# Performance work log

Measured on AMD Instinct MI355X. Metric: run time of the kernel, lower is better.

Reference implementation:

```python
import jax, jax.numpy as jnp
import numpy as np

C = 512
GROUPS = 32
EPS = 1e-6


def group_norm(x, w, b):
    # x: [B, C, H, W]
    B, Cc, H, W = x.shape
    xg = x.reshape(B, GROUPS, Cc // GROUPS, H, W)
    mean = xg.mean(axis=(2, 3, 4), keepdims=True)
    var = xg.var(axis=(2, 3, 4), keepdims=True)
    xg = (xg - mean) * jax.lax.rsqrt(var + EPS)
    x = xg.reshape(B, Cc, H, W)
    return x * w[None, :, None, None] + b[None, :, None, None]


def conv1x1(x, w, b):
    # 1x1 conv == per-pixel channel matmul; w: [Cout, Cin]
    return jnp.einsum('bchw,oc->bohw', x, w) + b[None, :, None, None]


def setup_inputs() -> dict:
    key = jax.random.key(0)
    ks = jax.random.split(key, 11)
    s = 1.0 / np.sqrt(C)
    d = {
        'x': jax.random.normal(ks[0], (2, C, 64, 64), dtype=jnp.float32),
        'gn_w': jnp.ones((C,), jnp.float32),
        'gn_b': jnp.zeros((C,), jnp.float32),
        'wq': jax.random.normal(ks[1], (C, C), jnp.float32) * s,
        'bq': jax.random.normal(ks[2], (C,), jnp.float32) * 0.01,
        'wk': jax.random.normal(ks[3], (C, C), jnp.float32) * s,
        'bk': jax.random.normal(ks[4], (C,), jnp.float32) * 0.01,
        'wv': jax.random.normal(ks[5], (C, C), jnp.float32) * s,
        'bv': jax.random.normal(ks[6], (C,), jnp.float32) * 0.01,
        'wo': jax.random.normal(ks[7], (C, C), jnp.float32) * s,
        'bo': jax.random.normal(ks[8], (C,), jnp.float32) * 0.01,
    }
    return d


def reference(x, gn_w, gn_b, wq, bq, wk, bk, wv, bv, wo, bo):
    B, Cc, H, W = x.shape
    h = group_norm(x, gn_w, gn_b)
    q = conv1x1(h, wq, bq)  # [B,C,H,W]
    k = conv1x1(h, wk, bk)
    v = conv1x1(h, wv, bv)
    N = H * W
    q = q.reshape(B, Cc, N).transpose(0, 2, 1)   # b n c
    k = k.reshape(B, Cc, N)                      # b c n
    v = v.reshape(B, Cc, N)                      # b c n
    attn = jnp.einsum('bic,bcj->bij', q, k) * (Cc ** -0.5)  # [B,N,N]
    attn = jax.nn.softmax(attn, axis=-1)
    # h_[b,c,i] = sum_j v[b,c,j] * attn[b,i,j]
    h_ = jnp.einsum('bcj,bij->bci', v, attn).reshape(B, Cc, H, W)
    h_ = conv1x1(h_, wo, bo)
    return x + h_
```

## Files before the change

### kernel.cpp

```cpp
#include <hip/hip_runtime.h>


typedef __attribute__((ext_vector_type(8))) short bf16x8;
typedef __attribute__((ext_vector_type(4))) float f32x4;
typedef unsigned short u16;
typedef unsigned int u32;

__device__ __forceinline__ u16 f2bf(float f) {
  u32 u = __builtin_bit_cast(u32, f);
  return (u16)((u + 0x7FFFu + ((u >> 16) & 1u)) >> 16);
}
__device__ __forceinline__ float bf2f(u16 u) {
  return __builtin_bit_cast(float, (u32)u << 16);
}
__device__ __forceinline__ void gll16(const void* g, void* l) {
  __builtin_amdgcn_global_load_lds((const __attribute__((address_space(1))) u32*)g,
                                   (__attribute__((address_space(3))) u32*)l, 16, 0, 0);
}

__global__ __launch_bounds__(256) void gn_stats(const float* __restrict__ x,
                                                float* __restrict__ stats) {
  int bg = blockIdx.x >> 3, slice = blockIdx.x & 7;
  const float4* xp = (const float4*)(x + (size_t)bg * 65536 + slice * 8192);
  int t = threadIdx.x;
  float s = 0.f, ss = 0.f;
  for (int i = t; i < 2048; i += 256) {
    float4 v = xp[i];
    s += v.x + v.y + v.z + v.w;
    ss += v.x * v.x + v.y * v.y + v.z * v.z + v.w * v.w;
  }
  for (int off = 32; off > 0; off >>= 1) {
    s += __shfl_down(s, off);
    ss += __shfl_down(ss, off);
  }
  __shared__ float rs[4], rss[4];
  if ((t & 63) == 0) { rs[t >> 6] = s; rss[t >> 6] = ss; }
  __syncthreads();
  if (t == 0) {
    atomicAdd(&stats[bg * 2 + 0], rs[0] + rs[1] + rs[2] + rs[3]);
    atomicAdd(&stats[bg * 2 + 1], rss[0] + rss[1] + rss[2] + rss[3]);
  }
}

__global__ __launch_bounds__(256) void gn_apply(
    const float* __restrict__ x, const float* __restrict__ w,
    const float* __restrict__ b, const float* __restrict__ stats,
    u16* __restrict__ ht) {
  int bg = blockIdx.x >> 3, slice = blockIdx.x & 7;
  int batch = bg >> 5, g = bg & 31;
  const float* xp = x + (size_t)bg * 65536;
  float mean = stats[bg * 2 + 0] * (1.f / 65536.f);
  float var = stats[bg * 2 + 1] * (1.f / 65536.f) - mean * mean;
  float rstd = rsqrtf(var + 1e-6f);
  float wsc[16], bsc[16];
#pragma unroll
  for (int cc = 0; cc < 16; ++cc) {
    float wv = w[g * 16 + cc];
    wsc[cc] = wv * rstd;
    bsc[cc] = b[g * 16 + cc] - mean * wsc[cc];
  }
  u16* hp = ht + (size_t)batch * 4096 * 512 + g * 16;
  int t = threadIdx.x;
  for (int n = slice * 512 + t; n < slice * 512 + 512; n += 256) {
    union { u16 pk[16]; uint4 v4[2]; } u;
#pragma unroll
    for (int cc = 0; cc < 16; ++cc)
      u.pk[cc] = f2bf(xp[cc * 4096 + n] * wsc[cc] + bsc[cc]);
    uint4* dst = (uint4*)(hp + (size_t)n * 512);
    dst[0] = u.v4[0];
    dst[1] = u.v4[1];
  }
}

__global__ __launch_bounds__(256) void wcvt_kernel(
    const float* __restrict__ wq, const float* __restrict__ wk,
    const float* __restrict__ wv, const float* __restrict__ wo,
    const float* __restrict__ bq, const float* __restrict__ bk,
    u16* __restrict__ Wqk, u16* __restrict__ Wv, u16* __restrict__ Wo,
    float* __restrict__ Bqk, float* __restrict__ stats,
    float* __restrict__ lsum) {
  int i = blockIdx.x * 256 + threadIdx.x;
  Wqk[i] = f2bf(wq[i]);
  Wqk[262144 + i] = f2bf(wk[i]);
  Wv[i] = f2bf(wv[i]);
  Wo[i] = f2bf(wo[i]);
  if (i < 512) { Bqk[i] = bq[i]; Bqk[512 + i] = bk[i]; }
  if (i < 128) stats[i] = 0.f;
  if (i < 8192) lsum[i] = 0.f;
}

template <int BM, int BN, int MODE>
__global__ __launch_bounds__(256) void mfma_gemm(
    const u16* __restrict__ A, int sA, const u16* __restrict__ B, int sB,
    int K, const float* __restrict__ bias, const float* __restrict__ res,
    void* __restrict__ out, int ostr, float scale,
    u16* __restrict__ p1, u16* __restrict__ p2, u16* __restrict__ p3,
    size_t zsA, size_t zsB, size_t zsO, float* __restrict__ lsum) {
  constexpr int TM = BM / 32, TN = BN / 32;
  constexpr int SIA = BM / 32, SIB = BN / 32;
  __shared__ char sm[(BM + BN) * 128];
  char* As = sm;
  char* Bs = sm + BM * 128;
  int t = threadIdx.x;
  int w = t >> 6, lane = t & 63, quad = lane >> 4, ln = lane & 15;
  int wm = w >> 1, wn = w & 1;
  int m0 = blockIdx.y * BM, n0 = blockIdx.x * BN;
  int zb, ksplit;
  if (MODE == 5) { zb = blockIdx.z >> 2; ksplit = blockIdx.z & 3; }
  else           { zb = blockIdx.z;      ksplit = 0; }
  const u16* Ab = A + (size_t)zb * zsA;
  const u16* Bb = B + (size_t)zb * zsB;
  int kbase = ksplit * K;
  f32x4 acc[TM][TN] = {};

  for (int k0 = 0; k0 < K; k0 += 64) {
#pragma unroll
    for (int si = 0; si < SIA; ++si) {
      int s = (w * SIA + si) * 64 + lane;
      gll16(Ab + (size_t)(m0 + (s & (BM - 1))) * sA + kbase + k0 + (s / BM) * 8,
            As + (w * SIA + si) * 1024);
    }
#pragma unroll
    for (int si = 0; si < SIB; ++si) {
      int s = (w * SIB + si) * 64 + lane;
      gll16(Bb + (size_t)(n0 + (s & (BN - 1))) * sB + kbase + k0 + (s / BN) * 8,
            Bs + (w * SIB + si) * 1024);
    }
    __syncthreads();
#pragma unroll
    for (int ks = 0; ks < 2; ++ks) {
      bf16x8 af[TM], bfr[TN];
#pragma unroll
      for (int tm = 0; tm < TM; ++tm)
        af[tm] = *(const bf16x8*)(As + (((ks * 4 + quad) * BM) + wm * (BM / 2) + tm * 16 + ln) * 16);
#pragma unroll
      for (int tn = 0; tn < TN; ++tn)
        bfr[tn] = *(const bf16x8*)(Bs + (((ks * 4 + quad) * BN) + wn * (BN / 2) + tn * 16 + ln) * 16);
#pragma unroll
      for (int tm = 0; tm < TM; ++tm)
#pragma unroll
        for (int tn = 0; tn < TN; ++tn)
          acc[tm][tn] = __builtin_amdgcn_mfma_f32_16x16x32_bf16(af[tm], bfr[tn], acc[tm][tn], 0, 0, 0);
    }
    __syncthreads();
  }

  u16* pdst = nullptr;
  if (MODE == 5) {
    pdst = (ksplit == 0) ? (u16*)out : (ksplit == 1) ? p1
         : (ksplit == 2) ? p2 : p3;
    pdst += (size_t)zb * zsO;
  } else if (MODE != 2) {
    pdst = (u16*)out + (size_t)zb * zsO;
  }

  if (MODE == 6) {
#pragma unroll
    for (int tm = 0; tm < TM; ++tm) {
#pragma unroll
      for (int r = 0; r < 4; ++r) {
        int m = m0 + wm * (BM / 2) + tm * 16 + quad * 4 + r;
        float rsum = 0.f;
#pragma unroll
        for (int tn = 0; tn < TN; ++tn) {
          int n = n0 + wn * (BN / 2) + tn * 16 + ln;
          float e = __expf(acc[tm][tn][r] * scale);
          rsum += e;
          pdst[(size_t)m * ostr + n] = f2bf(e);
        }
#pragma unroll
        for (int d = 1; d < 16; d <<= 1) rsum += __shfl_xor(rsum, d);
        if (ln == 0) atomicAdd(&lsum[(size_t)zb * 4096 + m], rsum);
      }
    }
    return;
  }

#pragma unroll
  for (int tm = 0; tm < TM; ++tm) {
    int mb = m0 + wm * (BM / 2) + tm * 16 + quad * 4;
#pragma unroll
    for (int tn = 0; tn < TN; ++tn) {
      int n = n0 + wn * (BN / 2) + tn * 16 + ln;
      float bn = (MODE == 0) ? bias[n] : 0.f;
#pragma unroll
      for (int r = 0; r < 4; ++r) {
        int m = mb + r;
        float v = acc[tm][tn][r];
        if (MODE == 0) {
          pdst[(size_t)m * ostr + n] = f2bf(v + bn);
        } else if (MODE == 1) {
          pdst[(size_t)m * ostr + n] = f2bf(v + bias[m]);
        } else if (MODE == 2) {
          int bb = n >> 12, nn = n & 4095;
          size_t off = ((size_t)(bb * 512 + m)) * 4096 + nn;
          ((float*)out)[off] = v + bias[m] + res[off];
        } else if (MODE == 3) {
          pdst[(size_t)m * ostr + n] = f2bf(v * scale);
        } else {
          pdst[(size_t)m * ostr + n] = f2bf(v);
        }
      }
    }
  }
}

__global__ __launch_bounds__(256) void softmax_kernel(u16* __restrict__ S) {
  u16* sp = S + (size_t)blockIdx.x * 4096;
  int t = threadIdx.x;
  int w = t >> 6;
  uint4 a = ((const uint4*)sp)[t * 2];
  uint4 b = ((const uint4*)sp)[t * 2 + 1];
  u32 words[8] = {a.x, a.y, a.z, a.w, b.x, b.y, b.z, b.w};
  float v[16];
#pragma unroll
  for (int i = 0; i < 8; ++i) {
    v[2 * i] = bf2f((u16)(words[i] & 0xFFFF));
    v[2 * i + 1] = bf2f((u16)(words[i] >> 16));
  }
  float mx = v[0];
#pragma unroll
  for (int i = 1; i < 16; ++i) mx = fmaxf(mx, v[i]);
#pragma unroll
  for (int d = 1; d < 64; d <<= 1) mx = fmaxf(mx, __shfl_xor(mx, d));
  __shared__ float red[8];
  if ((t & 63) == 0) red[w] = mx;
  __syncthreads();
  mx = fmaxf(fmaxf(red[0], red[1]), fmaxf(red[2], red[3]));
  float sum = 0.f;
#pragma unroll
  for (int i = 0; i < 16; ++i) {
    v[i] = __expf(v[i] - mx);
    sum += v[i];
  }
#pragma unroll
  for (int d = 1; d < 64; d <<= 1) sum += __shfl_xor(sum, d);
  if ((t & 63) == 0) red[4 + w] = sum;
  __syncthreads();
  float inv = 1.f / (red[4] + red[5] + red[6] + red[7]);
#pragma unroll
  for (int i = 0; i < 8; ++i)
    words[i] = (u32)f2bf(v[2 * i] * inv) | ((u32)f2bf(v[2 * i + 1] * inv) << 16);
  ((uint4*)sp)[t * 2] = make_uint4(words[0], words[1], words[2], words[3]);
  ((uint4*)sp)[t * 2 + 1] = make_uint4(words[4], words[5], words[6], words[7]);
}

template <bool NORM>
__global__ __launch_bounds__(256) void combine4_kernel(
    u16* __restrict__ P0, const u16* __restrict__ P1,
    const u16* __restrict__ P2, const u16* __restrict__ P3,
    const float* __restrict__ lsum) {
  int i = blockIdx.x * 256 + threadIdx.x;
  float inv = NORM ? 1.f / lsum[i >> 6] : 1.f;
  uint4 a = ((const uint4*)P0)[i];
  uint4 b = ((const uint4*)P1)[i];
  uint4 c = ((const uint4*)P2)[i];
  uint4 d = ((const uint4*)P3)[i];
  u32 wa[4] = {a.x, a.y, a.z, a.w}, wb[4] = {b.x, b.y, b.z, b.w};
  u32 wc[4] = {c.x, c.y, c.z, c.w}, wd[4] = {d.x, d.y, d.z, d.w};
  u32 wo_[4];
#pragma unroll
  for (int q = 0; q < 4; ++q) {
    float lo = bf2f((u16)(wa[q] & 0xFFFF)) + bf2f((u16)(wb[q] & 0xFFFF)) +
               bf2f((u16)(wc[q] & 0xFFFF)) + bf2f((u16)(wd[q] & 0xFFFF));
    float hi = bf2f((u16)(wa[q] >> 16)) + bf2f((u16)(wb[q] >> 16)) +
               bf2f((u16)(wc[q] >> 16)) + bf2f((u16)(wd[q] >> 16));
    wo_[q] = (u32)f2bf(lo * inv) | ((u32)f2bf(hi * inv) << 16);
  }
  ((uint4*)P0)[i] = make_uint4(wo_[0], wo_[1], wo_[2], wo_[3]);
}

extern "C" void kernel_launch(void* const* d_in, const int* in_sizes, int n_in,
                              void* d_out, int out_size, void* d_ws, size_t ws_size,
                              hipStream_t stream) {
  (void)in_sizes; (void)n_in; (void)out_size;
  const float* x = (const float*)d_in[0];
  const float* gnw = (const float*)d_in[1];
  const float* gnb = (const float*)d_in[2];
  const float* wq = (const float*)d_in[3];
  const float* bq = (const float*)d_in[4];
  const float* wk = (const float*)d_in[5];
  const float* bk = (const float*)d_in[6];
  const float* wv = (const float*)d_in[7];
  const float* bv = (const float*)d_in[8];
  const float* wo = (const float*)d_in[9];
  const float* bo = (const float*)d_in[10];
  float* out = (float*)d_out;

  const bool BIG = ws_size >= (size_t)96 * 1024 * 1024;
  char* ws = (char*)d_ws;
  u16* ht  = (u16*)(ws);
  u16* AOt = (u16*)(ws);
  u16* QKt = (u16*)(ws + 8388608);
  u16* S   = (u16*)(ws + 25165824);
  size_t woff = BIG ? 92274688u : 58720256u;
  u16* Wqk = (u16*)(ws + woff);
  u16* Wv  = (u16*)(ws + woff + 1048576);
  u16* Wo  = (u16*)(ws + woff + 1572864);
  float* stats = (float*)(ws + woff + 2097152);
  float* Bqk   = (float*)(ws + woff + 2097664);
  float* lsum  = (float*)(ws + woff + 2101760);
  u16* Vg  = (u16*)d_out;
  u16* P1g = (u16*)((char*)d_out + 8388608);

  wcvt_kernel<<<1024, 256, 0, stream>>>(wq, wk, wv, wo, bq, bk, Wqk, Wv, Wo,
                                        Bqk, stats, lsum);
  gn_stats<<<512, 256, 0, stream>>>(x, stats);
  gn_apply<<<512, 256, 0, stream>>>(x, gnw, gnb, stats, ht);
  mfma_gemm<128, 128, 0><<<dim3(8, 64), 256, 0, stream>>>(
      ht, 512, Wqk, 512, 512, Bqk, nullptr, QKt, 1024, 1.f,
      nullptr, nullptr, nullptr, 0, 0, 0, nullptr);
  mfma_gemm<64, 128, 1><<<dim3(64, 8), 256, 0, stream>>>(
      Wv, 512, ht, 512, 512, bv, nullptr, Vg, 8192, 1.f,
      nullptr, nullptr, nullptr, 0, 0, 0, nullptr);

  if (BIG) {
    mfma_gemm<128, 128, 6><<<dim3(32, 32, 2), 256, 0, stream>>>(
        QKt, 1024, QKt + 512, 1024, 512, nullptr, nullptr, S, 4096,
        0.044194173824159216f, nullptr, nullptr, nullptr,
        4194304u, 4194304u, 16777216u, lsum);
    mfma_gemm<128, 128, 5><<<dim3(4, 32, 8), 256, 0, stream>>>(
        S, 4096, Vg, 8192, 1024, nullptr, nullptr,
        AOt, 512, 1.f, P1g, QKt, QKt + 4194304, 16777216u, 4096u, 2097152u,
        nullptr);
    combine4_kernel<true><<<2048, 256, 0, stream>>>(
        AOt, P1g, QKt, QKt + 4194304, lsum);
  } else {
    u16* P2g = (u16*)((char*)d_out + 12582912);
    for (int b = 0; b < 2; ++b) {
      const u16* Qb = QKt + (size_t)b * 4194304;
      mfma_gemm<128, 128, 3><<<dim3(32, 32), 256, 0, stream>>>(
          Qb, 1024, Qb + 512, 1024, 512, nullptr, nullptr, S, 4096,
          0.044194173824159216f, nullptr, nullptr, nullptr, 0, 0, 0, nullptr);
      softmax_kernel<<<4096, 256, 0, stream>>>(S);
      u16* P0 = AOt + (size_t)b * 2097152;
      u16* P3 = QKt + (size_t)b * 4194304;
      mfma_gemm<128, 128, 5><<<dim3(4, 32, 4), 256, 0, stream>>>(
          S, 4096, Vg + (size_t)b * 4096, 8192, 1024, nullptr, nullptr,
          P0, 512, 1.f, P1g, P2g, P3, 0, 0, 0, nullptr);
      combine4_kernel<false><<<1024, 256, 0, stream>>>(P0, P1g, P2g, P3,
                                                       nullptr);
    }
  }
  mfma_gemm<64, 128, 2><<<dim3(64, 8), 256, 0, stream>>>(
      Wo, 512, AOt, 512, 512, bo, x, out, 0, 1.f,
      nullptr, nullptr, nullptr, 0, 0, 0, nullptr);
}
```

Measured before the change: 360.8 us.

## Fuse QK and V projection GEMMs into one launch and parameterize K-tile depth

Merges the QK projection GEMM and the V projection GEMM into a single MODE 7 launch of 768 blocks. The first 512 blocks compute QK with a column bias and the remaining 256 compute V with a row bias. It also adds a BK template parameter and uses a 32-deep K tile for the QK/V and score GEMMs, keeping 64 for the PV and output GEMMs. This saves one kernel launch and fills more CUs in one wave, but a smaller BK means more barriers per K iteration and less LDS staging per sync. The V blocks now use 128x128 tiles instead of 64x128.

```diff
diff --git a/kernel.cpp b/kernel.cpp
--- a/kernel.cpp
+++ b/kernel.cpp
@@ -89,7 +89,7 @@
   if (i < 8192) lsum[i] = 0.f;
 }
 
-template <int BM, int BN, int MODE>
+template <int BM, int BN, int BK, int MODE>
 __global__ __launch_bounds__(256) void mfma_gemm(
     const u16* __restrict__ A, int sA, const u16* __restrict__ B, int sB,
     int K, const float* __restrict__ bias, const float* __restrict__ res,
@@ -97,10 +97,11 @@
     u16* __restrict__ p1, u16* __restrict__ p2, u16* __restrict__ p3,
     size_t zsA, size_t zsB, size_t zsO, float* __restrict__ lsum) {
   constexpr int TM = BM / 32, TN = BN / 32;
-  constexpr int SIA = BM / 32, SIB = BN / 32;
-  __shared__ char sm[(BM + BN) * 128];
+  constexpr int SIA = BM * BK / 2048, SIB = BN * BK / 2048;
+  constexpr int KSTEPS = BK / 32;
+  __shared__ char sm[(BM + BN) * BK * 2];
   char* As = sm;
-  char* Bs = sm + BM * 128;
+  char* Bs = sm + BM * BK * 2;
   int t = threadIdx.x;
   int w = t >> 6, lane = t & 63, quad = lane >> 4, ln = lane & 15;
   int wm = w >> 1, wn = w & 1;
@@ -108,27 +109,44 @@
   int zb, ksplit;
   if (MODE == 5) { zb = blockIdx.z >> 2; ksplit = blockIdx.z & 3; }
   else           { zb = blockIdx.z;      ksplit = 0; }
-  const u16* Ab = A + (size_t)zb * zsA;
-  const u16* Bb = B + (size_t)zb * zsB;
+  const u16* Ab;
+  const u16* Bb;
+  int sAe = sA, sBe = sB;
+  bool qkPath = true;
+  if (MODE == 7) {
+    int bid = blockIdx.x;
+    if (bid < 512) {
+      Ab = A; Bb = B;
+      m0 = (bid >> 3) * 128; n0 = (bid & 7) * 128;
+    } else {
+      qkPath = false;
+      int b2 = bid - 512;
+      Ab = p2; sAe = 512; Bb = A; sBe = sA;
+      m0 = (b2 >> 6) * 128; n0 = (b2 & 63) * 128;
+    }
+  } else {
+    Ab = A + (size_t)zb * zsA;
+    Bb = B + (size_t)zb * zsB;
+  }
   int kbase = ksplit * K;
   f32x4 acc[TM][TN] = {};
 
-  for (int k0 = 0; k0 < K; k0 += 64) {
+  for (int k0 = 0; k0 < K; k0 += BK) {
 #pragma unroll
     for (int si = 0; si < SIA; ++si) {
       int s = (w * SIA + si) * 64 + lane;
-      gll16(Ab + (size_t)(m0 + (s & (BM - 1))) * sA + kbase + k0 + (s / BM) * 8,
+      gll16(Ab + (size_t)(m0 + (s & (BM - 1))) * sAe + kbase + k0 + (s / BM) * 8,
             As + (w * SIA + si) * 1024);
     }
 #pragma unroll
     for (int si = 0; si < SIB; ++si) {
       int s = (w * SIB + si) * 64 + lane;
-      gll16(Bb + (size_t)(n0 + (s & (BN - 1))) * sB + kbase + k0 + (s / BN) * 8,
+      gll16(Bb + (size_t)(n0 + (s & (BN - 1))) * sBe + kbase + k0 + (s / BN) * 8,
             Bs + (w * SIB + si) * 1024);
     }
     __syncthreads();
 #pragma unroll
-    for (int ks = 0; ks < 2; ++ks) {
+    for (int ks = 0; ks < KSTEPS; ++ks) {
       bf16x8 af[TM], bfr[TN];
 #pragma unroll
       for (int tm = 0; tm < TM; ++tm)
@@ -150,6 +168,8 @@
     pdst = (ksplit == 0) ? (u16*)out : (ksplit == 1) ? p1
          : (ksplit == 2) ? p2 : p3;
     pdst += (size_t)zb * zsO;
+  } else if (MODE == 7) {
+    pdst = qkPath ? (u16*)out : p1;
   } else if (MODE != 2) {
     pdst = (u16*)out + (size_t)zb * zsO;
   }
@@ -182,23 +202,21 @@
 #pragma unroll
     for (int tn = 0; tn < TN; ++tn) {
       int n = n0 + wn * (BN / 2) + tn * 16 + ln;
-      float bn = (MODE == 0) ? bias[n] : 0.f;
 #pragma unroll
       for (int r = 0; r < 4; ++r) {
         int m = mb + r;
         float v = acc[tm][tn][r];
-        if (MODE == 0) {
-          pdst[(size_t)m * ostr + n] = f2bf(v + bn);
-        } else if (MODE == 1) {
-          pdst[(size_t)m * ostr + n] = f2bf(v + bias[m]);
-        } else if (MODE == 2) {
+        if (MODE == 2) {
           int bb = n >> 12, nn = n & 4095;
           size_t off = ((size_t)(bb * 512 + m)) * 4096 + nn;
           ((float*)out)[off] = v + bias[m] + res[off];
         } else if (MODE == 3) {
           pdst[(size_t)m * ostr + n] = f2bf(v * scale);
-        } else {
+        } else if (MODE == 5 || MODE == 4) {
           pdst[(size_t)m * ostr + n] = f2bf(v);
+        } else if (MODE == 7) {
+          float bb = qkPath ? bias[n] : res[m];
+          pdst[(size_t)m * (qkPath ? ostr : 8192) + n] = f2bf(v + bb);
         }
       }
     }
@@ -307,19 +325,16 @@
                                         Bqk, stats, lsum);
   gn_stats<<<512, 256, 0, stream>>>(x, stats);
   gn_apply<<<512, 256, 0, stream>>>(x, gnw, gnb, stats, ht);
-  mfma_gemm<128, 128, 0><<<dim3(8, 64), 256, 0, stream>>>(
-      ht, 512, Wqk, 512, 512, Bqk, nullptr, QKt, 1024, 1.f,
-      nullptr, nullptr, nullptr, 0, 0, 0, nullptr);
-  mfma_gemm<64, 128, 1><<<dim3(64, 8), 256, 0, stream>>>(
-      Wv, 512, ht, 512, 512, bv, nullptr, Vg, 8192, 1.f,
-      nullptr, nullptr, nullptr, 0, 0, 0, nullptr);
+  mfma_gemm<128, 128, 32, 7><<<dim3(768), 256, 0, stream>>>(
+      ht, 512, Wqk, 512, 512, Bqk, bv, QKt, 1024, 1.f,
+      Vg, Wv, nullptr, 0, 0, 0, nullptr);
 
   if (BIG) {
-    mfma_gemm<128, 128, 6><<<dim3(32, 32, 2), 256, 0, stream>>>(
+    mfma_gemm<128, 128, 32, 6><<<dim3(32, 32, 2), 256, 0, stream>>>(
         QKt, 1024, QKt + 512, 1024, 512, nullptr, nullptr, S, 4096,
         0.044194173824159216f, nullptr, nullptr, nullptr,
         4194304u, 4194304u, 16777216u, lsum);
-    mfma_gemm<128, 128, 5><<<dim3(4, 32, 8), 256, 0, stream>>>(
+    mfma_gemm<128, 128, 64, 5><<<dim3(4, 32, 8), 256, 0, stream>>>(
         S, 4096, Vg, 8192, 1024, nullptr, nullptr,
         AOt, 512, 1.f, P1g, QKt, QKt + 4194304, 16777216u, 4096u, 2097152u,
         nullptr);
@@ -329,20 +344,20 @@
     u16* P2g = (u16*)((char*)d_out + 12582912);
     for (int b = 0; b < 2; ++b) {
       const u16* Qb = QKt + (size_t)b * 4194304;
-      mfma_gemm<128, 128, 3><<<dim3(32, 32), 256, 0, stream>>>(
+      mfma_gemm<128, 128, 32, 3><<<dim3(32, 32), 256, 0, stream>>>(
           Qb, 1024, Qb + 512, 1024, 512, nullptr, nullptr, S, 4096,
           0.044194173824159216f, nullptr, nullptr, nullptr, 0, 0, 0, nullptr);
       softmax_kernel<<<4096, 256, 0, stream>>>(S);
       u16* P0 = AOt + (size_t)b * 2097152;
       u16* P3 = QKt + (size_t)b * 4194304;
-      mfma_gemm<128, 128, 5><<<dim3(4, 32, 4), 256, 0, stream>>>(
+      mfma_gemm<128, 128, 64, 5><<<dim3(4, 32, 4), 256, 0, stream>>>(
           S, 4096, Vg + (size_t)b * 4096, 8192, 1024, nullptr, nullptr,
           P0, 512, 1.f, P1g, P2g, P3, 0, 0, 0, nullptr);
       combine4_kernel<false><<<1024, 256, 0, stream>>>(P0, P1g, P2g, P3,
                                                        nullptr);
     }
   }
-  mfma_gemm<64, 128, 2><<<dim3(64, 8), 256, 0, stream>>>(
+  mfma_gemm<64, 128, 64, 2><<<dim3(64, 8), 256, 0, stream>>>(
       Wo, 512, AOt, 512, 512, bo, x, out, 0, 1.f,
       nullptr, nullptr, nullptr, 0, 0, 0, nullptr);
 }
```

After: 362.9 us. Within noise of the previous version (+0.6%).
